# Kernel optimization log

Hardware: AMD Instinct MI355X
Metric: run time of the kernel (lower is better)

The kernel has to match this reference:

```python
import jax, jax.numpy as jnp
import numpy as np

BS, NSEQ, SPO_NSEQ, NUM_BOX, NUM_CTX, MAXC = 1024, 32, 32, 128, 5, 4


def _build_structure(seed=0):
    # Random trees over NSEQ nodes per sample: parent(i) = (i-1)//br, br in {2,3,4}.
    # adj[child, parent] = edge_id (as in the torch adj_matrices, -1 = no edge).
    rng = np.random.RandomState(seed)
    adjs = np.full((BS, NSEQ, NSEQ), -1, np.int64)
    trav = []
    for b in range(BS):
        br = rng.randint(2, 5)
        for i in range(1, NSEQ):
            adjs[b, i, (i - 1) // br] = i - 1  # edge ids < SPO_NSEQ
        trav.append(sorted(set(((np.arange(1, NSEQ) - 1) // br).tolist())))  # internal nodes, top-down
    L = max(len(t) for t in trav)
    padded = np.stack([np.pad(np.asarray(t), (L - len(t), 0), constant_values=-1) for t in trav])
    parent_idx = np.zeros((L, BS), np.int32)
    parent_valid = np.zeros((L, BS), np.float32)
    child_idx = np.zeros((L, BS, MAXC), np.int32)
    child_valid = np.zeros((L, BS, MAXC), np.float32)
    edge_idx = np.zeros((L, BS, MAXC), np.int32)
    flat_sample = np.zeros((L, BS), np.int32)
    flat_slot = np.zeros((L, BS), np.int32)
    for it in range(L):
        pairs = []  # flat children ordering: sample 0's children, then sample 1's, ...
        for b in range(BS):
            p = int(padded[b, it])
            ch = np.nonzero(adjs[b, :, p] != -1)[0] if p != -1 else np.array([], np.int64)
            if p == -1 or len(ch) == 0:
                pairs.append((b, 0))  # dummy child 0, masked out (no_parent_or_no_children=0)
            else:
                parent_idx[it, b] = p
                parent_valid[it, b] = 1.0
                for j, c in enumerate(ch):
                    child_idx[it, b, j] = c
                    child_valid[it, b, j] = 1.0
                    edge_idx[it, b, j] = adjs[b, c, p]
                pairs.extend((b, j) for j in range(len(ch)))
        for f in range(BS):  # flat row f used as update_mask[sampid] in the torch code
            flat_sample[it, f], flat_slot[it, f] = pairs[f]
    return parent_idx, parent_valid, child_idx, child_valid, edge_idx, flat_sample, flat_slot


def setup_inputs() -> dict:
    key = jax.random.key(0)
    ks = jax.random.split(key, 6)
    pi, pv, ci, cv, ei, fs, fl = _build_structure()
    ent_attn = jax.random.normal(ks[0], (BS, NSEQ, NUM_BOX), jnp.float32)
    spo_attn = jax.random.normal(ks[1], (BS, SPO_NSEQ, NUM_BOX, NUM_CTX), jnp.float32)
    base = jax.random.randint(ks[2], (BS, SPO_NSEQ, NUM_BOX), 0, NUM_BOX)
    # distinct ctx indices per (b, e, box) slot so the scatter has no duplicate columns
    ctx_idx_adjusted = ((base[..., None] + jnp.arange(NUM_CTX, dtype=jnp.int32) * 7) % NUM_BOX).astype(jnp.int32)
    roi_mask = (jax.random.uniform(ks[3], (BS, SPO_NSEQ, NUM_BOX, NUM_CTX)) < 0.9).astype(jnp.float32)
    roi_cls = jax.random.randint(ks[4], (BS, NUM_BOX), -1, 20).astype(jnp.int32)
    weight_on_children = jax.random.uniform(ks[5], (BS, NSEQ, NUM_BOX), dtype=jnp.float32)
    return dict(ent_attn=ent_attn, spo_attn=spo_attn, ctx_idx_adjusted=ctx_idx_adjusted,
                roi_mask=roi_mask, roi_cls=roi_cls, weight_on_children=weight_on_children,
                parent_idx=jnp.asarray(pi), parent_valid=jnp.asarray(pv),
                child_idx=jnp.asarray(ci), child_valid=jnp.asarray(cv),
                edge_idx=jnp.asarray(ei), flat_sample=jnp.asarray(fs), flat_slot=jnp.asarray(fl))


def _propagate(ent_attn, spo_attn, roi_mask, weight_on_children,
               ctx_idx_adjusted, roi_cls,
               parent_idx, parent_valid, child_idx, child_valid, edge_idx, flat_sample, flat_slot):
    bs, nseq, nbox = ent_attn.shape
    bar = jnp.arange(bs)
    cls_mask = (roi_cls != -1).astype(ent_attn.dtype)            # [bs, nbox]
    L = parent_idx.shape[0]                                      # tree depth (small, static)
    for it in range(L):
        pidx, pval = parent_idx[it], parent_valid[it]            # [bs]
        cidx, cval, eidx = child_idx[it], child_valid[it], edge_idx[it]  # [bs, C]
        # selected_children_atn: [bs, C, nbox]
        ch_atn = ent_attn[bar[:, None], cidx] * cval[..., None] * cls_mask[:, None, :]
        # per-edge gathers + transpose(1,2): [bs, spo, nbox, ctx] -> [bs, C, ctx, nbox]
        gather_T = lambda t: jnp.swapaxes(t[bar[:, None], eidx], -1, -2)
        k_ctx = gather_T(ctx_idx_adjusted)                       # int indices
        m_roi = gather_T(roi_mask)
        filt = m_roi * cval[..., None, None]                     # filter_mask
        k_scores = gather_T(spo_attn) * filt * cls_mask[:, None, None, :]
        # sgmn transfer: sum over boxes -> [bs, C, ctx]
        transfer = jnp.sum(ch_atn[:, :, None, :] * k_scores * m_roi, axis=-1) + 1e-6
        # faithful to torch quirk: value row = first child of sample (cnt), index row = flat row sampid
        upd_cols = k_ctx[flat_sample[it], flat_slot[it], :, 0]   # [bs, ctx] box indices
        add_to_sub = jnp.full((bs, nbox), 1e-6, ent_attn.dtype).at[bar[:, None], upd_cols].set(transfer[:, 0, :])
        sub_atn = ent_attn[bar, pidx]                            # [bs, nbox]
        upd = sub_atn + add_to_sub * weight_on_children[bar, pidx]   # opt='add'
        # NormAttnMap (cossim): norm = max(|x|) detached, clamped >= 1
        norm = jax.lax.stop_gradient(jnp.max(jnp.abs(upd), axis=-1, keepdims=True))
        upd = upd / jnp.where(norm <= 1, jnp.ones_like(norm), norm)
        upd = jnp.where(roi_cls == -1, -1.0, upd)                # opt 'add' -> -1
        new_rows = jnp.where(pval[:, None] > 0, upd, sub_atn)    # only write where bs_mask
        ent_attn = ent_attn.at[bar, pidx].set(new_rows)
    return ent_attn


def reference(ent_attn, spo_attn, ctx_idx_adjusted, roi_mask, roi_cls, weight_on_children,
              parent_idx, parent_valid, child_idx, child_valid, edge_idx, flat_sample, flat_slot):
    return _propagate(ent_attn, spo_attn, roi_mask, weight_on_children,
                      ctx_idx_adjusted, roi_cls,
                      parent_idx, parent_valid, child_idx, child_valid, edge_idx, flat_sample, flat_slot)
```

## Files before the change

### kernel.cpp

```cpp
#include <hip/hip_runtime.h>

constexpr int kBS   = 1024;
constexpr int kNSEQ = 32;
constexpr int kNBOX = 128;
constexpr int kNCTX = 5;
constexpr int kMAXC = 4;

__global__ __launch_bounds__(128) void fused_propagate(
    const float* __restrict__ ent,
    const float* __restrict__ spo,
    const int*   __restrict__ ctx,
    const float* __restrict__ roi,
    const int*   __restrict__ cls,
    const float* __restrict__ woc,
    const int*   __restrict__ pidx,
    const float* __restrict__ pval,
    const int*   __restrict__ cidx,
    const int*   __restrict__ eidx,
    const int*   __restrict__ fsamp,
    const int*   __restrict__ fslot,
    float* __restrict__ out,
    int L)
{
    const int b   = blockIdx.x;
    const int row = blockIdx.y;
    const int k   = threadIdx.x;
    const int rb  = (b * kNSEQ + row) * kNBOX + k;

    int it = -1;
    for (int i = 0; i < L; ++i) {
        const int j = i * kBS + b;
        if (pval[j] > 0.0f && pidx[j] == row) { it = i; break; }
    }
    if (it < 0) {
        out[rb] = ent[rb];
        return;
    }

    const int idx = it * kBS + b;
    const int c0  = cidx[idx * kMAXC];
    const int e0  = eidx[idx * kMAXC];
    const int fs  = fsamp[idx];
    const int fl  = fslot[idx];
    const int ep  = eidx[(it * kBS + fs) * kMAXC + fl];

    const int   clsk = cls[b * kNBOX + k];
    const float cm   = (clsk != -1) ? 1.0f : 0.0f;
    const float a    = ent[(b * kNSEQ + c0) * kNBOX + k] * cm;

    const size_t sb = ((size_t)(b * kNSEQ + e0) * kNBOX + k) * kNCTX;
    float part[kNCTX];
    #pragma unroll
    for (int c = 0; c < kNCTX; ++c)
        part[c] = a * spo[sb + c] * roi[sb + c];

    #pragma unroll
    for (int off = 32; off >= 1; off >>= 1) {
        #pragma unroll
        for (int c = 0; c < kNCTX; ++c)
            part[c] += __shfl_xor(part[c], off, 64);
    }
    __shared__ float wsum[2][kNCTX];
    __shared__ float wmax[2];
    const int wave = k >> 6;
    if ((k & 63) == 0) {
        #pragma unroll
        for (int c = 0; c < kNCTX; ++c) wsum[wave][c] = part[c];
    }
    __syncthreads();
    float t[kNCTX];
    #pragma unroll
    for (int c = 0; c < kNCTX; ++c) t[c] = wsum[0][c] + wsum[1][c] + 1e-6f;

    const int cbase = (fs * kNSEQ + ep) * kNBOX * kNCTX;
    float val = 1e-6f;
    #pragma unroll
    for (int c = 0; c < kNCTX; ++c) {
        if (ctx[cbase + c] == k) val = t[c];
    }

    float upd = ent[rb] + val * woc[rb];

    float m = fabsf(upd);
    #pragma unroll
    for (int off = 32; off >= 1; off >>= 1)
        m = fmaxf(m, __shfl_xor(m, off, 64));
    if ((k & 63) == 0) wmax[wave] = m;
    __syncthreads();
    const float norm = fmaxf(wmax[0], wmax[1]);
    if (norm > 1.0f) upd /= norm;
    if (clsk == -1) upd = -1.0f;
    out[rb] = upd;
}

extern "C" void kernel_launch(void* const* d_in, const int* in_sizes, int n_in,
                              void* d_out, int out_size, void* d_ws, size_t ws_size,
                              hipStream_t stream) {
    const float* ent   = (const float*)d_in[0];
    const float* spo   = (const float*)d_in[1];
    const int*   ctx   = (const int*)  d_in[2];
    const float* roi   = (const float*)d_in[3];
    const int*   cls   = (const int*)  d_in[4];
    const float* woc   = (const float*)d_in[5];
    const int*   pidx  = (const int*)  d_in[6];
    const float* pval  = (const float*)d_in[7];
    const int*   cidx  = (const int*)  d_in[8];
    const int*   eidx  = (const int*)  d_in[10];
    const int*   fsamp = (const int*)  d_in[11];
    const int*   fslot = (const int*)  d_in[12];
    float* out = (float*)d_out;

    const int L = in_sizes[6] / kBS;

    fused_propagate<<<dim3(kBS, kNSEQ), dim3(128), 0, stream>>>(
        ent, spo, ctx, roi, cls, woc, pidx, pval, cidx, eidx, fsamp, fslot, out, L);
}
```

Measured before the change: 262.1 us.

## Map one wave per row with two elements per lane and shared parent lookup

Each block now handles 16 rows of one sample, with a wave processing 4 rows and each lane covering two box elements. Because a whole row fits in one wave, the cross-wave shared-memory reductions and barriers are gone. The per-row linear search over iterations is replaced by one shared table built once per block. The change also cuts the block count from 32K to 2K and uses float2 loads. In exchange there is less parallelism per block, and if a row is a parent in several iterations the table keeps the last iteration instead of the first.

```diff
diff --git a/kernel.cpp b/kernel.cpp
--- a/kernel.cpp
+++ b/kernel.cpp
@@ -6,7 +6,7 @@
 constexpr int kNCTX = 5;
 constexpr int kMAXC = 4;
 
-__global__ __launch_bounds__(128) void fused_propagate(
+__global__ __launch_bounds__(256) void fused_propagate(
     const float* __restrict__ ent,
     const float* __restrict__ spo,
     const int*   __restrict__ ctx,
@@ -22,75 +22,83 @@
     float* __restrict__ out,
     int L)
 {
-    const int b   = blockIdx.x;
-    const int row = blockIdx.y;
-    const int k   = threadIdx.x;
-    const int rb  = (b * kNSEQ + row) * kNBOX + k;
+    const int b    = blockIdx.x;
+    const int half = blockIdx.y;
+    const int tid  = threadIdx.x;
+    const int lane = tid & 63;
+    const int wave = tid >> 6;
 
-    int it = -1;
-    for (int i = 0; i < L; ++i) {
-        const int j = i * kBS + b;
-        if (pval[j] > 0.0f && pidx[j] == row) { it = i; break; }
+    __shared__ int rowit[kNSEQ];
+    if (wave == 0) {
+        if (lane < kNSEQ) rowit[lane] = -1;
+        for (int i = lane; i < L; i += 64) {
+            const int j = i * kBS + b;
+            if (pval[j] > 0.0f) rowit[pidx[j]] = i;
+        }
     }
-    if (it < 0) {
-        out[rb] = ent[rb];
-        return;
-    }
+    __syncthreads();
 
-    const int idx = it * kBS + b;
-    const int c0  = cidx[idx * kMAXC];
-    const int e0  = eidx[idx * kMAXC];
-    const int fs  = fsamp[idx];
-    const int fl  = fslot[idx];
-    const int ep  = eidx[(it * kBS + fs) * kMAXC + fl];
-
-    const int   clsk = cls[b * kNBOX + k];
-    const float cm   = (clsk != -1) ? 1.0f : 0.0f;
-    const float a    = ent[(b * kNSEQ + c0) * kNBOX + k] * cm;
-
-    const size_t sb = ((size_t)(b * kNSEQ + e0) * kNBOX + k) * kNCTX;
-    float part[kNCTX];
-    #pragma unroll
-    for (int c = 0; c < kNCTX; ++c)
-        part[c] = a * spo[sb + c] * roi[sb + c];
+    const int  k0   = 2 * lane, k1 = k0 + 1;
+    const int2 clsv = *(const int2*)&cls[b * kNBOX + k0];
 
     #pragma unroll
-    for (int off = 32; off >= 1; off >>= 1) {
+    for (int r = 0; r < 4; ++r) {
+        const int row = half * 16 + wave * 4 + r;
+        const int rb  = (b * kNSEQ + row) * kNBOX;
+        const int it  = rowit[row];
+        if (it < 0) {
+            *(float2*)&out[rb + k0] = *(const float2*)&ent[rb + k0];
+            continue;
+        }
+        const int idx = it * kBS + b;
+        const int c0  = cidx[idx * kMAXC];
+        const int e0  = eidx[idx * kMAXC];
+        const int fs  = fsamp[idx];
+        const int fl  = fslot[idx];
+        const int ep  = eidx[(it * kBS + fs) * kMAXC + fl];
+
+        const float2 av = *(const float2*)&ent[(b * kNSEQ + c0) * kNBOX + k0];
+        const float a0 = (clsv.x != -1) ? av.x : 0.0f;
+        const float a1 = (clsv.y != -1) ? av.y : 0.0f;
+
+        const size_t sbase = ((size_t)(b * kNSEQ + e0) * kNBOX + k0) * kNCTX;
+        float part[kNCTX];
         #pragma unroll
         for (int c = 0; c < kNCTX; ++c)
-            part[c] += __shfl_xor(part[c], off, 64);
+            part[c] = a0 * spo[sbase + c]         * roi[sbase + c]
+                    + a1 * spo[sbase + kNCTX + c] * roi[sbase + kNCTX + c];
+
+        #pragma unroll
+        for (int off = 32; off >= 1; off >>= 1) {
+            #pragma unroll
+            for (int c = 0; c < kNCTX; ++c)
+                part[c] += __shfl_xor(part[c], off, 64);
+        }
+
+        const int cbase = (fs * kNSEQ + ep) * kNBOX * kNCTX;
+        float val0 = 1e-6f, val1 = 1e-6f;
+        #pragma unroll
+        for (int c = 0; c < kNCTX; ++c) {
+            const int   cc = ctx[cbase + c];
+            const float tc = part[c] + 1e-6f;
+            if (cc == k0) val0 = tc;
+            if (cc == k1) val1 = tc;
+        }
+
+        const float2 ev = *(const float2*)&ent[rb + k0];
+        const float2 wv = *(const float2*)&woc[rb + k0];
+        float u0 = ev.x + val0 * wv.x;
+        float u1 = ev.y + val1 * wv.y;
+
+        float m = fmaxf(fabsf(u0), fabsf(u1));
+        #pragma unroll
+        for (int off = 32; off >= 1; off >>= 1)
+            m = fmaxf(m, __shfl_xor(m, off, 64));
+        if (m > 1.0f) { u0 /= m; u1 /= m; }
+        if (clsv.x == -1) u0 = -1.0f;
+        if (clsv.y == -1) u1 = -1.0f;
+        *(float2*)&out[rb + k0] = make_float2(u0, u1);
     }
-    __shared__ float wsum[2][kNCTX];
-    __shared__ float wmax[2];
-    const int wave = k >> 6;
-    if ((k & 63) == 0) {
-        #pragma unroll
-        for (int c = 0; c < kNCTX; ++c) wsum[wave][c] = part[c];
-    }
-    __syncthreads();
-    float t[kNCTX];
-    #pragma unroll
-    for (int c = 0; c < kNCTX; ++c) t[c] = wsum[0][c] + wsum[1][c] + 1e-6f;
-
-    const int cbase = (fs * kNSEQ + ep) * kNBOX * kNCTX;
-    float val = 1e-6f;
-    #pragma unroll
-    for (int c = 0; c < kNCTX; ++c) {
-        if (ctx[cbase + c] == k) val = t[c];
-    }
-
-    float upd = ent[rb] + val * woc[rb];
-
-    float m = fabsf(upd);
-    #pragma unroll
-    for (int off = 32; off >= 1; off >>= 1)
-        m = fmaxf(m, __shfl_xor(m, off, 64));
-    if ((k & 63) == 0) wmax[wave] = m;
-    __syncthreads();
-    const float norm = fmaxf(wmax[0], wmax[1]);
-    if (norm > 1.0f) upd /= norm;
-    if (clsk == -1) upd = -1.0f;
-    out[rb] = upd;
 }
 
 extern "C" void kernel_launch(void* const* d_in, const int* in_sizes, int n_in,
@@ -112,6 +120,6 @@
 
     const int L = in_sizes[6] / kBS;
 
-    fused_propagate<<<dim3(kBS, kNSEQ), dim3(128), 0, stream>>>(
+    fused_propagate<<<dim3(kBS, 2), dim3(256), 0, stream>>>(
         ent, spo, ctx, roi, cls, woc, pidx, pval, cidx, eidx, fsamp, fslot, out, L);
 }
```

Result: faster. 240.9 us (-8.1%).
